# Optimization experiments

Measured on AMD Instinct MI355X. Metric: run time of the kernel, lower is better.

The kernel has to match this reference:

```python
import jax, jax.numpy as jnp
import numpy as np

TEMP = 1.0  # temperature

def setup_inputs() -> dict:
    key = jax.random.key(0)
    ks = jax.random.split(key, 16)
    B, Cin, Cout, H, W, K, kk, A = 32, 64, 64, 128, 128, 4, 3, 16
    c_ = Cin + Cout
    r = lambda k, s: jax.random.normal(k, s, dtype=jnp.float32)
    return {
        'x': r(ks[0], (B, Cin, H, W)),
        'fc_w': r(ks[1], (A, Cin)) * 0.1,
        'ch_w': r(ks[2], (Cin, A)) * 0.1,
        'ch_b': jnp.zeros((Cin,), jnp.float32),
        'f_w': r(ks[3], (Cout, A)) * 0.1,
        'f_b': jnp.zeros((Cout,), jnp.float32),
        'sp_w': r(ks[4], (kk * kk, A)) * 0.1,
        'sp_b': jnp.zeros((kk * kk,), jnp.float32),
        'k_w': r(ks[5], (K, A)) * 0.1,
        'k_b': jnp.zeros((K,), jnp.float32),
        'fus_w1': r(ks[6], (c_ // 16, c_)) * 0.1,
        'fus_b1': jnp.zeros((c_ // 16,), jnp.float32),
        'fus_w2': r(ks[7], (c_, c_ // 16)) * 0.1,
        'fus_b2': jnp.zeros((c_,), jnp.float32),
        'weight': r(ks[8], (K, Cout, Cin, kk, kk)) * (1.0 / np.sqrt(Cin * kk * kk)),
    }

def reference(x, fc_w, ch_w, ch_b, f_w, f_b, sp_w, sp_b, k_w, k_b,
              fus_w1, fus_b1, fus_w2, fus_b2, weight):
    B, Cin, H, W = x.shape
    K, Cout, _, kk, _ = weight.shape
    # --- Attention branches (on globally pooled features) ---
    pooled = x.mean(axis=(2, 3))                      # (B, Cin)
    a = jax.nn.relu(pooled @ fc_w.T)                  # (B, A)
    ch_att = jax.nn.sigmoid(a @ ch_w.T + ch_b)        # (B, Cin)
    f_att = jax.nn.sigmoid(a @ f_w.T + f_b)           # (B, Cout)
    sp_att = jax.nn.sigmoid(a @ sp_w.T + sp_b).reshape(B, 1, 1, 1, kk, kk)
    k_att = jax.nn.softmax((a @ k_w.T + k_b) / TEMP, axis=1).reshape(B, K, 1, 1, 1, 1)
    # --- Attention fusion ---
    att = jnp.concatenate([ch_att, f_att], axis=1)    # (B, Cin+Cout)
    att2 = jax.nn.sigmoid(jax.nn.relu(att @ fus_w1.T + fus_b1) @ fus_w2.T + fus_b2)
    s1 = att2[:, :Cin].sum(axis=1)
    s2 = att2[:, Cin:].sum(axis=1)
    score = jax.nn.softmax(jnp.stack([s1, s2], axis=1) / TEMP, axis=1)
    w1 = score[:, 0][:, None, None, None]
    w2 = score[:, 1][:, None, None, None]
    # --- Apply channel attention, aggregate per-sample weights ---
    xm = w1 * x * ch_att[:, :, None, None]
    # (B,K,1,1,kk,kk)*(B,K,1,1,1,1)*(1,K,Cout,Cin,kk,kk) summed over K
    agg_w = (sp_att * k_att * weight[None]).sum(axis=1)  # (B, Cout, Cin, kk, kk)
    # --- Per-sample conv2d (stride 1, padding 1) ---
    def conv_one(xb, wb):
        return jax.lax.conv_general_dilated(
            xb[None], wb, window_strides=(1, 1), padding=[(1, 1), (1, 1)],
            dimension_numbers=('NCHW', 'OIHW', 'NCHW'))[0]
    out = jax.vmap(conv_one)(xm, agg_w)               # (B, Cout, H, W)
    return w2 * out * f_att[:, :, None, None]
```

## Files before the change

### kernel.cpp

```cpp
#include <hip/hip_runtime.h>
#include <math.h>
#include <stdint.h>

typedef short bf16x8 __attribute__((ext_vector_type(8)));
typedef float f32x16 __attribute__((ext_vector_type(16)));
typedef unsigned short ushort_t;

#define WS_POOLED 0
#define WS_CIN    2048
#define WS_COUT   4096
#define WS_SP9    6144
#define WS_K4     6432
#define WS_WF     8192

static __device__ __forceinline__ unsigned f2bf(float f) {
  unsigned u = __builtin_bit_cast(unsigned, f);
  return (u + 0x7FFFu + ((u >> 16) & 1u)) >> 16;
}

__global__ __launch_bounds__(256) void pool_kernel(const float* __restrict__ x,
                                                   float* __restrict__ pooled) {
  const int bc = blockIdx.x;
  const int tid = threadIdx.x;
  const float4* p = (const float4*)(x + (size_t)bc * 16384);
  float s = 0.f;
  for (int j = tid; j < 4096; j += 256) {
    float4 v = p[j];
    s += (v.x + v.y) + (v.z + v.w);
  }
#pragma unroll
  for (int off = 32; off > 0; off >>= 1) s += __shfl_down(s, off, 64);
  __shared__ float red[4];
  if ((tid & 63) == 0) red[tid >> 6] = s;
  __syncthreads();
  if (tid == 0) pooled[bc] = (red[0] + red[1] + red[2] + red[3]) * (1.f / 16384.f);
}

__global__ __launch_bounds__(128) void att_kernel(
    const float* __restrict__ pooled,
    const float* __restrict__ fc_w, const float* __restrict__ ch_w, const float* __restrict__ ch_b,
    const float* __restrict__ f_w,  const float* __restrict__ f_b,
    const float* __restrict__ sp_w, const float* __restrict__ sp_b,
    const float* __restrict__ k_w,  const float* __restrict__ k_b,
    const float* __restrict__ fus_w1, const float* __restrict__ fus_b1,
    const float* __restrict__ fus_w2, const float* __restrict__ fus_b2,
    float* __restrict__ o_cin, float* __restrict__ o_cout,
    float* __restrict__ o_sp9, float* __restrict__ o_k4) {
  const int b = blockIdx.x;
  const int t = threadIdx.x;
  __shared__ float s_pool[64], s_a[16], s_att[128], s_sp[9], s_k[4], s_h[8],
      s_att2[128], s_red[2], s_w12[2];

  if (t < 64) s_pool[t] = pooled[b * 64 + t];
  __syncthreads();

  if (t < 16) {
    float s = 0.f;
    for (int c = 0; c < 64; ++c) s += s_pool[c] * fc_w[t * 64 + c];
    s_a[t] = fmaxf(s, 0.f);
  }
  __syncthreads();

  if (t < 64) {
    float s = ch_b[t];
    for (int j = 0; j < 16; ++j) s += s_a[j] * ch_w[t * 16 + j];
    s_att[t] = 1.f / (1.f + expf(-s));
  } else {
    const int o = t - 64;
    float s = f_b[o];
    for (int j = 0; j < 16; ++j) s += s_a[j] * f_w[o * 16 + j];
    s_att[t] = 1.f / (1.f + expf(-s));
  }
  if (t < 9) {
    float s = sp_b[t];
    for (int j = 0; j < 16; ++j) s += s_a[j] * sp_w[t * 16 + j];
    s_sp[t] = 1.f / (1.f + expf(-s));
  }
  if (t < 4) {
    float s = k_b[t];
    for (int j = 0; j < 16; ++j) s += s_a[j] * k_w[t * 16 + j];
    s_k[t] = s;
  }
  __syncthreads();

  if (t < 8) {
    float s = fus_b1[t];
    for (int c = 0; c < 128; ++c) s += s_att[c] * fus_w1[t * 128 + c];
    s_h[t] = fmaxf(s, 0.f);
  }
  if (t == 127) {
    float m = fmaxf(fmaxf(s_k[0], s_k[1]), fmaxf(s_k[2], s_k[3]));
    float e0 = expf(s_k[0] - m), e1 = expf(s_k[1] - m);
    float e2 = expf(s_k[2] - m), e3 = expf(s_k[3] - m);
    float inv = 1.f / (e0 + e1 + e2 + e3);
    s_k[0] = e0 * inv; s_k[1] = e1 * inv; s_k[2] = e2 * inv; s_k[3] = e3 * inv;
  }
  __syncthreads();

  {
    float s = fus_b2[t];
    for (int j = 0; j < 8; ++j) s += s_h[j] * fus_w2[t * 8 + j];
    s_att2[t] = 1.f / (1.f + expf(-s));
  }
  __syncthreads();

  if (t < 2) {
    float s = 0.f;
    for (int c = 0; c < 64; ++c) s += s_att2[t * 64 + c];
    s_red[t] = s;
  }
  __syncthreads();
  if (t == 0) {
    float m = fmaxf(s_red[0], s_red[1]);
    float e1 = expf(s_red[0] - m), e2 = expf(s_red[1] - m);
    float inv = 1.f / (e1 + e2);
    s_w12[0] = e1 * inv;
    s_w12[1] = e2 * inv;
  }
  __syncthreads();

  if (t < 64) {
    o_cin[b * 64 + t]  = s_w12[0] * s_att[t];
    o_cout[b * 64 + t] = s_w12[1] * s_att[64 + t];
  }
  if (t < 9) o_sp9[b * 9 + t] = s_sp[t];
  if (t < 4) o_k4[b * 4 + t] = s_k[t];
}

__global__ __launch_bounds__(256) void wf_kernel(const float* __restrict__ weight,
                                                 const float* __restrict__ cin,
                                                 const float* __restrict__ cout_,
                                                 const float* __restrict__ sp9,
                                                 const float* __restrict__ k4,
                                                 ushort_t* __restrict__ wfb) {
  const int bo = blockIdx.x;
  const int b = bo >> 6, o = bo & 63;
  const float co = cout_[b * 64 + o];
  const float k0 = k4[b * 4 + 0], k1 = k4[b * 4 + 1];
  const float k2 = k4[b * 4 + 2], k3 = k4[b * 4 + 3];
  for (int idx = threadIdx.x; idx < 576; idx += 256) {
    const int pq = idx >> 6, i = idx & 63;
    const size_t wi = ((size_t)o * 64 + i) * 9 + pq;
    float s = k0 * weight[wi] + k1 * weight[36864 + wi] +
              k2 * weight[73728 + wi] + k3 * weight[110592 + wi];
    float v = co * sp9[b * 9 + pq] * cin[b * 64 + i] * s;
    wfb[((size_t)(b * 9 + pq) * 64 + o) * 64 + i] = (ushort_t)f2bf(v);
  }
}

__global__ __launch_bounds__(512, 4) void conv_kernel(const float* __restrict__ x,
                                                      const ushort_t* __restrict__ wfb,
                                                      float* __restrict__ out) {
  const int b  = blockIdx.x >> 5;
  const int h0 = (blockIdx.x & 31) << 2;
  const int tid = threadIdx.x;
  const int lane = tid & 63;
  const int wid = tid >> 6;
  const int rw = wid >> 1;
  const int obase = (wid & 1) << 5;
  const int l31 = lane & 31;
  const int hi = lane >> 5;

  __shared__ __align__(16) short sx[816 * 16];

  f32x16 acc[4];
#pragma unroll
  for (int nt = 0; nt < 4; ++nt)
#pragma unroll
    for (int r = 0; r < 16; ++r) acc[nt][r] = 0.f;

  const ushort_t* wfb_b = wfb + (size_t)b * 9 * 64 * 64;

  const bool sactive = tid < 408;
  int so = 0, sr = 0, sc = 0;
  if (sactive) { so = tid / 204; const int rem = tid % 204; sr = rem / 34; sc = rem % 34; }
  const int gr  = h0 - 1 + sr;
  const int gcb = sc * 4 - 4;
  const bool inb = sactive && ((unsigned)gr < 128u) && ((unsigned)gcb < 128u);
  const int pixb = sr * 136 + sc * 4;
  const int key = ((pixb >> 2) & 7) << 4;
  const float* xrow = x + ((size_t)(b * 64) * 16384) + gr * 128 + gcb;

  for (int ch = 0; ch < 4; ++ch) {
    __syncthreads();
    if (inb) {
      const int c0 = ch * 16 + so * 8;
      float4 v[8];
#pragma unroll
      for (int j = 0; j < 8; ++j)
        v[j] = *(const float4*)(xrow + (size_t)(c0 + j) * 16384);
#pragma unroll
      for (int j = 0; j < 4; ++j) {
        uint4 u;
        u.x = f2bf(((const float*)&v[0])[j]) | (f2bf(((const float*)&v[1])[j]) << 16);
        u.y = f2bf(((const float*)&v[2])[j]) | (f2bf(((const float*)&v[3])[j]) << 16);
        u.z = f2bf(((const float*)&v[4])[j]) | (f2bf(((const float*)&v[5])[j]) << 16);
        u.w = f2bf(((const float*)&v[6])[j]) | (f2bf(((const float*)&v[7])[j]) << 16);
        *(uint4*)((char*)sx + ((((pixb + j) * 32) + so * 16) ^ key)) = u;
      }
    } else if (sactive) {
      const uint4 z = make_uint4(0u, 0u, 0u, 0u);
#pragma unroll
      for (int j = 0; j < 4; ++j)
        *(uint4*)((char*)sx + ((((pixb + j) * 32) + so * 16) ^ key)) = z;
    }
    __syncthreads();

#pragma unroll
    for (int p = 0; p < 3; ++p) {
#pragma unroll
      for (int q = 0; q < 3; ++q) {
        const int tap = p * 3 + q;
        bf16x8 af = *(const bf16x8*)(wfb_b + ((tap * 64 + obase + l31) * 64) + ch * 16 + hi * 8);
#pragma unroll
        for (int nt = 0; nt < 4; ++nt) {
          const int pix = (rw + p) * 136 + 3 + q + nt * 32 + l31;
          const int boff = ((pix * 32) + hi * 16) ^ (((pix >> 2) & 7) << 4);
          bf16x8 bf = *(const bf16x8*)((const char*)sx + boff);
          acc[nt] = __builtin_amdgcn_mfma_f32_32x32x16_bf16(af, bf, acc[nt], 0, 0, 0);
        }
      }
    }
  }

  const int h = h0 + rw;
#pragma unroll
  for (int nt = 0; nt < 4; ++nt) {
    const int col = nt * 32 + l31;
#pragma unroll
    for (int reg = 0; reg < 16; ++reg) {
      const int o = obase + (reg & 3) + ((reg >> 2) << 3) + (hi << 2);
      out[(((size_t)(b * 64 + o)) * 128 + h) * 128 + col] = acc[nt][reg];
    }
  }
}

extern "C" void kernel_launch(void* const* d_in, const int* in_sizes, int n_in,
                              void* d_out, int out_size, void* d_ws, size_t ws_size,
                              hipStream_t stream) {
  const float* x      = (const float*)d_in[0];
  const float* fc_w   = (const float*)d_in[1];
  const float* ch_w   = (const float*)d_in[2];
  const float* ch_b   = (const float*)d_in[3];
  const float* f_w    = (const float*)d_in[4];
  const float* f_b    = (const float*)d_in[5];
  const float* sp_w   = (const float*)d_in[6];
  const float* sp_b   = (const float*)d_in[7];
  const float* k_w    = (const float*)d_in[8];
  const float* k_b    = (const float*)d_in[9];
  const float* fus_w1 = (const float*)d_in[10];
  const float* fus_b1 = (const float*)d_in[11];
  const float* fus_w2 = (const float*)d_in[12];
  const float* fus_b2 = (const float*)d_in[13];
  const float* weight = (const float*)d_in[14];
  float* ws  = (float*)d_ws;
  float* out = (float*)d_out;
  ushort_t* wfb = (ushort_t*)(ws + WS_WF);

  pool_kernel<<<2048, 256, 0, stream>>>(x, ws + WS_POOLED);
  att_kernel<<<32, 128, 0, stream>>>(ws + WS_POOLED, fc_w, ch_w, ch_b, f_w, f_b,
                                     sp_w, sp_b, k_w, k_b, fus_w1, fus_b1,
                                     fus_w2, fus_b2, ws + WS_CIN, ws + WS_COUT,
                                     ws + WS_SP9, ws + WS_K4);
  wf_kernel<<<2048, 256, 0, stream>>>(weight, ws + WS_CIN, ws + WS_COUT,
                                      ws + WS_SP9, ws + WS_K4, wfb);
  conv_kernel<<<1024, 512, 0, stream>>>(x, wfb, out);
}
```

Measured before the change: 146.1 us.

## Double-buffer conv input tiles and give each wave both output-channel halves

The conv kernel now uses 256 threads where each wave computes all 64 output channels for one row, so every B-fragment read from shared memory feeds two MFMAs. Input staging is double-buffered: the next 16-channel chunk of x is loaded into registers during the MFMAs on the current chunk, then packed into the other buffer, which halves the number of barriers. The intent is to hide global load latency and cut LDS traffic per MFMA. In exchange it uses twice the LDS, about twice the accumulator registers (launch bounds drop to 2 blocks), and fewer threads do the global loads.

```diff
diff --git a/kernel.cpp b/kernel.cpp
--- a/kernel.cpp
+++ b/kernel.cpp
@@ -16,6 +16,9 @@
 static __device__ __forceinline__ unsigned f2bf(float f) {
   unsigned u = __builtin_bit_cast(unsigned, f);
   return (u + 0x7FFFu + ((u >> 16) & 1u)) >> 16;
+}
+static __device__ __forceinline__ unsigned pk2(float a, float b) {
+  return f2bf(a) | (f2bf(b) << 16);
 }
 
 __global__ __launch_bounds__(256) void pool_kernel(const float* __restrict__ x,
@@ -148,91 +151,119 @@
   }
 }
 
-__global__ __launch_bounds__(512, 4) void conv_kernel(const float* __restrict__ x,
+#define CONV_BUF_BYTES 26112
+__global__ __launch_bounds__(256, 2) void conv_kernel(const float* __restrict__ x,
                                                       const ushort_t* __restrict__ wfb,
                                                       float* __restrict__ out) {
   const int b  = blockIdx.x >> 5;
   const int h0 = (blockIdx.x & 31) << 2;
   const int tid = threadIdx.x;
   const int lane = tid & 63;
-  const int wid = tid >> 6;
-  const int rw = wid >> 1;
-  const int obase = (wid & 1) << 5;
+  const int wv  = tid >> 6;
   const int l31 = lane & 31;
-  const int hi = lane >> 5;
-
-  __shared__ __align__(16) short sx[816 * 16];
-
-  f32x16 acc[4];
-#pragma unroll
-  for (int nt = 0; nt < 4; ++nt)
-#pragma unroll
-    for (int r = 0; r < 16; ++r) acc[nt][r] = 0.f;
+  const int hi  = lane >> 5;
+
+  __shared__ __align__(16) short sx[2 * 816 * 16];
+
+  f32x16 acc[2][4];
+#pragma unroll
+  for (int of = 0; of < 2; ++of)
+#pragma unroll
+    for (int nt = 0; nt < 4; ++nt)
+#pragma unroll
+      for (int r = 0; r < 16; ++r) acc[of][nt][r] = 0.f;
 
   const ushort_t* wfb_b = wfb + (size_t)b * 9 * 64 * 64;
 
-  const bool sactive = tid < 408;
-  int so = 0, sr = 0, sc = 0;
-  if (sactive) { so = tid / 204; const int rem = tid % 204; sr = rem / 34; sc = rem % 34; }
+  const bool sact = tid < 204;
+  const int sr = tid / 34, sc = tid % 34;
   const int gr  = h0 - 1 + sr;
   const int gcb = sc * 4 - 4;
-  const bool inb = sactive && ((unsigned)gr < 128u) && ((unsigned)gcb < 128u);
+  const bool inb = sact && ((unsigned)gr < 128u) && ((unsigned)gcb < 128u);
   const int pixb = sr * 136 + sc * 4;
-  const int key = ((pixb >> 2) & 7) << 4;
-  const float* xrow = x + ((size_t)(b * 64) * 16384) + gr * 128 + gcb;
-
+  const int key = (tid & 7) << 4;
+  const float* xrow = x + ((size_t)b * 64) * 16384 + gr * 128 + gcb;
+
+#define PACK_WRITE(BUFB)                                                        \
+  do {                                                                          \
+    _Pragma("unroll") for (int oct = 0; oct < 2; ++oct) {                       \
+      _Pragma("unroll") for (int j = 0; j < 4; ++j) {                           \
+        uint4 u;                                                                \
+        u.x = pk2(((const float*)&v[oct * 8 + 0])[j], ((const float*)&v[oct * 8 + 1])[j]); \
+        u.y = pk2(((const float*)&v[oct * 8 + 2])[j], ((const float*)&v[oct * 8 + 3])[j]); \
+        u.z = pk2(((const float*)&v[oct * 8 + 4])[j], ((const float*)&v[oct * 8 + 5])[j]); \
+        u.w = pk2(((const float*)&v[oct * 8 + 6])[j], ((const float*)&v[oct * 8 + 7])[j]); \
+        *(uint4*)((char*)sx + (BUFB) + ((((pixb + j) * 32) + oct * 16) ^ key)) = u; \
+      }                                                                         \
+    }                                                                           \
+  } while (0)
+
+  if (sact && !inb) {
+    const uint4 z = make_uint4(0u, 0u, 0u, 0u);
+#pragma unroll
+    for (int buf = 0; buf < 2; ++buf)
+#pragma unroll
+      for (int oct = 0; oct < 2; ++oct)
+#pragma unroll
+        for (int j = 0; j < 4; ++j)
+          *(uint4*)((char*)sx + buf * CONV_BUF_BYTES +
+                    ((((pixb + j) * 32) + oct * 16) ^ key)) = z;
+  }
+
+  float4 v[16];
+  if (inb) {
+#pragma unroll
+    for (int ci = 0; ci < 16; ++ci) v[ci] = *(const float4*)(xrow + (size_t)ci * 16384);
+    PACK_WRITE(0);
+  }
+  __syncthreads();
+
+#pragma unroll
   for (int ch = 0; ch < 4; ++ch) {
-    __syncthreads();
-    if (inb) {
-      const int c0 = ch * 16 + so * 8;
-      float4 v[8];
-#pragma unroll
-      for (int j = 0; j < 8; ++j)
-        v[j] = *(const float4*)(xrow + (size_t)(c0 + j) * 16384);
-#pragma unroll
-      for (int j = 0; j < 4; ++j) {
-        uint4 u;
-        u.x = f2bf(((const float*)&v[0])[j]) | (f2bf(((const float*)&v[1])[j]) << 16);
-        u.y = f2bf(((const float*)&v[2])[j]) | (f2bf(((const float*)&v[3])[j]) << 16);
-        u.z = f2bf(((const float*)&v[4])[j]) | (f2bf(((const float*)&v[5])[j]) << 16);
-        u.w = f2bf(((const float*)&v[6])[j]) | (f2bf(((const float*)&v[7])[j]) << 16);
-        *(uint4*)((char*)sx + ((((pixb + j) * 32) + so * 16) ^ key)) = u;
-      }
-    } else if (sactive) {
-      const uint4 z = make_uint4(0u, 0u, 0u, 0u);
-#pragma unroll
-      for (int j = 0; j < 4; ++j)
-        *(uint4*)((char*)sx + ((((pixb + j) * 32) + so * 16) ^ key)) = z;
-    }
-    __syncthreads();
-
+    const int c0 = ch * 16;
+    if (ch < 3 && inb) {
+#pragma unroll
+      for (int ci = 0; ci < 16; ++ci)
+        v[ci] = *(const float4*)(xrow + (size_t)(c0 + 16 + ci) * 16384);
+    }
+    const int bufb = (ch & 1) * CONV_BUF_BYTES;
 #pragma unroll
     for (int p = 0; p < 3; ++p) {
 #pragma unroll
       for (int q = 0; q < 3; ++q) {
         const int tap = p * 3 + q;
-        bf16x8 af = *(const bf16x8*)(wfb_b + ((tap * 64 + obase + l31) * 64) + ch * 16 + hi * 8);
+        bf16x8 af0 = *(const bf16x8*)(wfb_b + (tap * 64 + l31) * 64 + c0 + hi * 8);
+        bf16x8 af1 = *(const bf16x8*)(wfb_b + (tap * 64 + 32 + l31) * 64 + c0 + hi * 8);
 #pragma unroll
         for (int nt = 0; nt < 4; ++nt) {
-          const int pix = (rw + p) * 136 + 3 + q + nt * 32 + l31;
-          const int boff = ((pix * 32) + hi * 16) ^ (((pix >> 2) & 7) << 4);
+          const int pix = (wv + p) * 136 + 3 + q + nt * 32 + l31;
+          const int boff = bufb + ((pix * 32 + hi * 16) ^ (((pix >> 2) & 7) << 4));
           bf16x8 bf = *(const bf16x8*)((const char*)sx + boff);
-          acc[nt] = __builtin_amdgcn_mfma_f32_32x32x16_bf16(af, bf, acc[nt], 0, 0, 0);
+          acc[0][nt] = __builtin_amdgcn_mfma_f32_32x32x16_bf16(af0, bf, acc[0][nt], 0, 0, 0);
+          acc[1][nt] = __builtin_amdgcn_mfma_f32_32x32x16_bf16(af1, bf, acc[1][nt], 0, 0, 0);
         }
       }
     }
-  }
-
-  const int h = h0 + rw;
-#pragma unroll
-  for (int nt = 0; nt < 4; ++nt) {
-    const int col = nt * 32 + l31;
-#pragma unroll
-    for (int reg = 0; reg < 16; ++reg) {
-      const int o = obase + (reg & 3) + ((reg >> 2) << 3) + (hi << 2);
-      out[(((size_t)(b * 64 + o)) * 128 + h) * 128 + col] = acc[nt][reg];
-    }
-  }
+    if (ch < 3) {
+      if (inb) PACK_WRITE(((ch + 1) & 1) * CONV_BUF_BYTES);
+      __syncthreads();
+    }
+  }
+
+  const int h = h0 + wv;
+#pragma unroll
+  for (int of = 0; of < 2; ++of) {
+#pragma unroll
+    for (int nt = 0; nt < 4; ++nt) {
+      const int col = nt * 32 + l31;
+#pragma unroll
+      for (int reg = 0; reg < 16; ++reg) {
+        const int o = of * 32 + (reg & 3) + ((reg >> 2) << 3) + (hi << 2);
+        out[(((size_t)(b * 64 + o)) * 128 + h) * 128 + col] = acc[of][nt][reg];
+      }
+    }
+  }
+#undef PACK_WRITE
 }
 
 extern "C" void kernel_launch(void* const* d_in, const int* in_sizes, int n_in,
@@ -264,5 +295,5 @@
                                      ws + WS_SP9, ws + WS_K4);
   wf_kernel<<<2048, 256, 0, stream>>>(weight, ws + WS_CIN, ws + WS_COUT,
                                       ws + WS_SP9, ws + WS_K4, wfb);
-  conv_kernel<<<1024, 512, 0, stream>>>(x, wfb, out);
-}
+  conv_kernel<<<1024, 256, 0, stream>>>(x, wfb, out);
+}
```

Result: slower. 170.1 us (+16.5%).
